# Kernel tuning notes

Hardware: AMD Instinct MI355X
Metric: run time of the kernel (lower is better)

The kernel has to match this reference:

```python
import math
import jax, jax.numpy as jnp
import numpy as np

LOG_NORM = -0.5 * math.log(2.0 * math.pi)  # per-dim gaussian normalizer
HEADS = 4
EM_ITERS = 5


def _mab(x, wq, bq, wk, bk, wv, bv, wo, bo):
    # Set-Transformer SAB(x) = MAB(x, x), ln=False
    B, S, D = x.shape
    dh = D // HEADS
    q = (x @ wq + bq).reshape(B, S, HEADS, dh)
    k = (x @ wk + bk).reshape(B, S, HEADS, dh)
    v = (x @ wv + bv).reshape(B, S, HEADS, dh)
    att = jax.nn.softmax(jnp.einsum('bqhd,bkhd->bhqk', q, k) / math.sqrt(D), axis=-1)
    o = q + jnp.einsum('bhqk,bkhd->bqhd', att, v)
    o = o.reshape(B, S, D)
    return o + jax.nn.relu(o @ wo + bo)


def setup_inputs() -> dict:
    key = jax.random.key(0)
    ks = jax.random.split(key, 16)
    B, S, D, L, K, MC = 16, 256, 512, 64, 20, 10
    s512 = 1.0 / math.sqrt(512.0)
    inp = {
        'H': jax.random.normal(ks[0], (B, S, D), jnp.float32),
        'eps': jax.random.normal(ks[1], (B * S, MC, L), jnp.float32),
        'sab_wq': jax.random.normal(ks[2], (2, D, D), jnp.float32) * s512,
        'sab_bq': jnp.zeros((2, D), jnp.float32),
        'sab_wk': jax.random.normal(ks[3], (2, D, D), jnp.float32) * s512,
        'sab_bk': jnp.zeros((2, D), jnp.float32),
        'sab_wv': jax.random.normal(ks[4], (2, D, D), jnp.float32) * s512,
        'sab_bv': jnp.zeros((2, D), jnp.float32),
        'sab_wo': jax.random.normal(ks[5], (2, D, D), jnp.float32) * s512,
        'sab_bo': jnp.zeros((2, D), jnp.float32),
        'wz': jax.random.normal(ks[6], (D, 2 * L), jnp.float32) * 0.02,
        'bz': jnp.zeros((2 * L,), jnp.float32),
        'w1': jax.random.normal(ks[7], (L, 2 * D), jnp.float32) * (1.0 / math.sqrt(L)),
        'b1': jnp.zeros((2 * D,), jnp.float32),
        'w2': jax.random.normal(ks[8], (2 * D, 2 * D), jnp.float32) * (1.0 / math.sqrt(2 * D)),
        'b2': jnp.zeros((2 * D,), jnp.float32),
        'w3': jax.random.normal(ks[9], (2 * D, D), jnp.float32) * (1.0 / math.sqrt(2 * D)),
        'b3': jnp.zeros((D,), jnp.float32),
    }
    rng = np.random.default_rng(1)
    # component_size distinct indices into the S*MC latent samples, per batch
    inp['init_idx'] = jnp.asarray(
        np.stack([rng.permutation(S * MC)[:K] for _ in range(B)]).astype(np.int32))
    return inp


def reference(H, eps, init_idx, sab_wq, sab_bq, sab_wk, sab_bk, sab_wv, sab_bv,
              sab_wo, sab_bo, wz, bz, w1, b1, w2, b2, w3, b3):
    B, S, D = H.shape
    MC, L = eps.shape[1], eps.shape[2]
    K = init_idx.shape[1]

    # q(z|x): two SABs + linear head
    h = H
    for i in range(2):
        h = _mab(h, sab_wq[i], sab_bq[i], sab_wk[i], sab_bk[i],
                 sab_wv[i], sab_bv[i], sab_wo[i], sab_bo[i])
    stats = h @ wz + bz                                    # [B,S,2L]
    mean, logvar = stats[..., :L], stats[..., L:]
    std = jnp.exp(0.5 * logvar)
    z = mean.reshape(B * S, 1, L) + eps * std.reshape(B * S, 1, L)
    z = z.reshape(B, S, MC, L)
    all_z = z.reshape(B, S * MC, L)                        # [B,N,L]

    # unsupervised EM prior (unit-variance GMM); distances via expansion
    pi = jnp.full((B, K), 1.0 / K, dtype=H.dtype)
    mu = jnp.take_along_axis(all_z, init_idx[:, :, None], axis=1)  # [B,K,L]
    x2 = jnp.sum(all_z * all_z, axis=-1)                   # [B,N]
    for _ in range(EM_ITERS):
        m2 = jnp.sum(mu * mu, axis=-1)                     # [B,K]
        ll = (-0.5 * (x2[:, :, None] - 2.0 * jnp.einsum('bnd,bkd->bnk', all_z, mu)
                      + m2[:, None, :]) + L * LOG_NORM + jnp.log(pi)[:, None, :])
        post = jax.nn.softmax(ll, axis=-1)                 # [B,N,K]
        Nk = post.sum(axis=1)                              # [B,K]
        pi = Nk / Nk.sum(axis=-1, keepdims=True)
        mu = jnp.einsum('bnk,bnd->bkd', post, all_z) / Nk[:, :, None]
    pi = jax.lax.stop_gradient(pi)
    mu = jax.lax.stop_gradient(mu)

    # reconstruction
    zf = z.reshape(-1, L)
    hr = jax.nn.relu(zf @ w1 + b1)
    hr = jax.nn.relu(hr @ w2 + b2)
    hr = jax.nn.relu(hr @ w3 + b3)
    hr = hr.reshape(B, S, MC, D)
    rec_loss = jnp.sum((hr - H[:, :, None, :]) ** 2) / (B * S * MC)

    # KL
    log_qz = jnp.sum(-0.5 * (logvar[:, :, None, :]
                             + (z - mean[:, :, None, :]) ** 2 / jnp.exp(logvar)[:, :, None, :])
                     + LOG_NORM, axis=-1)                  # [B,S,MC]
    z2 = jnp.sum(z * z, axis=-1)                           # [B,S,MC]
    m2 = jnp.sum(mu * mu, axis=-1)                         # [B,K]
    ll = (-0.5 * (z2[..., None] - 2.0 * jnp.einsum('bsmd,bkd->bsmk', z, mu)
                  + m2[:, None, None, :]) + L * LOG_NORM + jnp.log(pi)[:, None, None, :])
    log_pz = jax.scipy.special.logsumexp(ll, axis=-1)      # [B,S,MC]
    kl_loss = jnp.mean(log_qz - log_pz)
    return rec_loss, kl_loss
```

## Files before the change

kernel.cpp:

```cpp
#include <hip/hip_runtime.h>
#include <hip/hip_bf16.h>
#include <math.h>


#define BATCH 16
#define SEQ 256
#define DIM 512
#define NH 4
#define DH 128
#define LD 64
#define KC 20
#define MC 10
#define NPTS 2560
#define BS_TOT 4096
#define NROWS 40960
#define LOG_NORM (-0.9189385332046727f)

typedef __attribute__((ext_vector_type(8))) short bf16x8;
typedef __attribute__((ext_vector_type(4))) float f32x4;
typedef __hip_bfloat16 bf;

__device__ inline float warpReduceSum(float v) {
    for (int o = 32; o > 0; o >>= 1) v += __shfl_down(v, o);
    return v;
}

__device__ inline void async_copy16(const bf* g, bf* l) {
    __builtin_amdgcn_global_load_lds(
        (const __attribute__((address_space(1))) unsigned int*)g,
        (__attribute__((address_space(3))) unsigned int*)l, 16, 0, 0);
}

__device__ inline void split_store(float x, bf* ph, bf* pl, long idx) {
    const bf h = __float2bfloat16(x);
    ph[idx] = h;
    pl[idx] = __float2bfloat16(x - __bfloat162float(h));
}

template<int MODE>
__global__ __launch_bounds__(256, 3)
void gemm3t(const bf* __restrict__ Ah, const bf* __restrict__ Al,
            const bf* __restrict__ Bh, const bf* __restrict__ Bl,
            int K, int lda, int ldb,
            const float* __restrict__ b0, const float* __restrict__ b1v,
            const float* __restrict__ b2v,
            float* __restrict__ outF,
            bf* __restrict__ P1h, bf* __restrict__ P1l,
            bf* __restrict__ P2h, bf* __restrict__ P2l,
            bf* __restrict__ P3h, bf* __restrict__ P3l,
            const bf* __restrict__ Rh, const bf* __restrict__ Rl)
{
    __shared__ __align__(16) char smem[49152];
    float* Xs = (float*)smem;

    const int t = threadIdx.x;
    const int m0 = blockIdx.y * 64, n0 = blockIdx.x * 128;
    const int w = t >> 6, lane = t & 63;
    const int wn = w * 32;
    const int fm = lane & 15, quad = lane >> 4, fk = quad * 8;
    const int srow = t >> 2, scol = (t & 3) * 8;

    f32x4 acc[4][2];
#pragma unroll
    for (int i = 0; i < 4; i++)
#pragma unroll
        for (int j = 0; j < 2; j++) acc[i][j] = (f32x4){0.f, 0.f, 0.f, 0.f};

    const int nk2 = K >> 6;
    for (int kk2 = 0; kk2 < nk2; kk2++) {
#pragma unroll
        for (int h = 0; h < 2; h++) {
            const int kk = kk2 * 2 + h;
            char* base = smem + h * 24576;
            bf* Ash = (bf*)base;
            bf* Asl = (bf*)(base + 4096);
            bf* Bsh = (bf*)(base + 8192);
            bf* Bsl = (bf*)(base + 16384);
            const long ao = (long)(m0 + srow) * lda + kk * 32 + scol;
            const long bo = (long)(n0 + srow) * ldb + kk * 32 + scol;
            async_copy16(Ah + ao, Ash + w * 512);
            async_copy16(Al + ao, Asl + w * 512);
            async_copy16(Bh + bo, Bsh + w * 512);
            async_copy16(Bh + bo + 64L * ldb, Bsh + 2048 + w * 512);
            async_copy16(Bl + bo, Bsl + w * 512);
            async_copy16(Bl + bo + 64L * ldb, Bsl + 2048 + w * 512);
        }
        __syncthreads();

#pragma unroll
        for (int h = 0; h < 2; h++) {
            char* base = smem + h * 24576;
            bf* Ash = (bf*)base;
            bf* Asl = (bf*)(base + 4096);
            bf* Bsh = (bf*)(base + 8192);
            bf* Bsl = (bf*)(base + 16384);
            bf16x8 afh[4], afl[4], bfh[2], bfl[2];
#pragma unroll
            for (int mi = 0; mi < 4; mi++) {
                afh[mi] = *(const bf16x8*)&Ash[(mi * 16 + fm) * 32 + fk];
                afl[mi] = *(const bf16x8*)&Asl[(mi * 16 + fm) * 32 + fk];
            }
#pragma unroll
            for (int ni = 0; ni < 2; ni++) {
                bfh[ni] = *(const bf16x8*)&Bsh[(wn + ni * 16 + fm) * 32 + fk];
                bfl[ni] = *(const bf16x8*)&Bsl[(wn + ni * 16 + fm) * 32 + fk];
            }
#pragma unroll
            for (int mi = 0; mi < 4; mi++)
#pragma unroll
                for (int ni = 0; ni < 2; ni++) {
                    acc[mi][ni] = __builtin_amdgcn_mfma_f32_16x16x32_bf16(
                        afh[mi], bfh[ni], acc[mi][ni], 0, 0, 0);
                    acc[mi][ni] = __builtin_amdgcn_mfma_f32_16x16x32_bf16(
                        afh[mi], bfl[ni], acc[mi][ni], 0, 0, 0);
                    acc[mi][ni] = __builtin_amdgcn_mfma_f32_16x16x32_bf16(
                        afl[mi], bfh[ni], acc[mi][ni], 0, 0, 0);
                }
        }
        __syncthreads();
    }

    const int rl = t >> 2;
    const int cc4 = (t & 3) * 16;

    for (int p = 0; p < 2; p++) {
        if ((w >> 1) == p) {
            const int cb = wn - p * 64;
#pragma unroll
            for (int mi = 0; mi < 4; mi++)
#pragma unroll
                for (int ni = 0; ni < 2; ni++) {
                    const int c = cb + ni * 16 + fm;
#pragma unroll
                    for (int r = 0; r < 4; r++)
                        Xs[(mi * 16 + quad * 4 + r) * 68 + c] = acc[mi][ni][r];
                }
        }
        __syncthreads();

        if (MODE == 0 && n0 >= 1024) {
            const int hh = (n0 >> 7) & 3;
            const int dd = p * 64 + rl;
            const int bb = m0 >> 8;
            const int sb = (m0 & 255) + cc4;
            const float bias = b2v[hh * 128 + dd];
            const long ob = (((long)(bb * NH + hh) * DH + dd) << 8) + sb;
#pragma unroll
            for (int j = 0; j < 2; j++) {
                bf16x8 vh, vl;
#pragma unroll
                for (int i = 0; i < 8; i++) {
                    const float x = Xs[(cc4 + j * 8 + i) * 68 + rl] + bias;
                    const bf h = __float2bfloat16(x);
                    vh[i] = *(const short*)&h;
                    const bf l = __float2bfloat16(x - __bfloat162float(h));
                    vl[i] = *(const short*)&l;
                }
                *(bf16x8*)&P3h[ob + j * 8] = vh;
                *(bf16x8*)&P3l[ob + j * 8] = vl;
            }
        } else {
            float xv[16];
#pragma unroll
            for (int i = 0; i < 4; i++)
                *(float4*)&xv[i * 4] = *(const float4*)&Xs[rl * 68 + cc4 + i * 4];

            if (MODE == 0) {
                const int which = n0 >> 9;
                const int colq = (n0 & 511) + p * 64 + cc4;
                const float* bias = which ? b1v : b0;
                bf* Ph = which ? P2h : P1h;
                bf* Pl = which ? P2l : P1l;
                const long ob = (long)(m0 + rl) * 512 + colq;
#pragma unroll
                for (int j = 0; j < 2; j++) {
                    bf16x8 vh, vl;
#pragma unroll
                    for (int i = 0; i < 8; i++) {
                        const float x = xv[j * 8 + i] + bias[colq + j * 8 + i];
                        const bf h = __float2bfloat16(x); vh[i] = *(const short*)&h;
                        const bf l = __float2bfloat16(x - __bfloat162float(h));
                        vl[i] = *(const short*)&l;
                    }
                    *(bf16x8*)&Ph[ob + j * 8] = vh;
                    *(bf16x8*)&Pl[ob + j * 8] = vl;
                }
            } else if (MODE == 3) {
                const int colg = n0 + p * 64 + cc4;
                const long ob = (long)(m0 + rl) * 512 + colg;
#pragma unroll
                for (int j = 0; j < 2; j++) {
                    const bf16x8 rh = *(const bf16x8*)&Rh[ob + j * 8];
                    const bf16x8 rv = *(const bf16x8*)&Rl[ob + j * 8];
                    bf16x8 vh, vl;
#pragma unroll
                    for (int i = 0; i < 8; i++) {
                        short sh = rh[i], sl = rv[i];
                        float x = fmaxf(xv[j * 8 + i] + b0[colg + j * 8 + i], 0.f)
                                + __bfloat162float(*(const bf*)&sh)
                                + __bfloat162float(*(const bf*)&sl);
                        const bf h = __float2bfloat16(x); vh[i] = *(const short*)&h;
                        const bf l = __float2bfloat16(x - __bfloat162float(h));
                        vl[i] = *(const short*)&l;
                    }
                    *(bf16x8*)&P1h[ob + j * 8] = vh;
                    *(bf16x8*)&P1l[ob + j * 8] = vl;
                }
            } else {
                const int colg = p * 64 + cc4;
                const long ob = (long)(m0 + rl) * 128 + colg;
#pragma unroll
                for (int i = 0; i < 4; i++) {
                    float4 v = *(float4*)&xv[i * 4];
                    v.x += b0[colg + i * 4 + 0];
                    v.y += b0[colg + i * 4 + 1];
                    v.z += b0[colg + i * 4 + 2];
                    v.w += b0[colg + i * 4 + 3];
                    *(float4*)&outF[ob + i * 4] = v;
                }
            }
        }
        __syncthreads();
    }
}

__global__ __launch_bounds__(256)
void attn_fused(const bf* __restrict__ qh, const bf* __restrict__ ql,
                const bf* __restrict__ kh, const bf* __restrict__ kl,
                const bf* __restrict__ vTh, const bf* __restrict__ vTl,
                bf* __restrict__ oh, bf* __restrict__ ol)
{
    __shared__ __align__(16) char smem[43008];
    bf* Qsh = (bf*)smem;            bf* Qsl = (bf*)(smem + 4096);
    bf* Ksh = (bf*)(smem + 8192);   bf* Ksl = (bf*)(smem + 24576);
    bf* Psh = (bf*)smem;            bf* Psl = (bf*)(smem + 4096);
    bf* Vsh = (bf*)(smem + 8192);   bf* Vsl = (bf*)(smem + 16384);
    float (*red)[4]  = (float(*)[4])(smem + 40960);
    float (*red2)[4] = (float(*)[4])(smem + 41984);

    const int t = threadIdx.x;
    const int z = blockIdx.y;
    const int m0 = blockIdx.x * 64;
    const int bb = z >> 2, hh = z & 3;
    const long hOff = (long)bb * 131072 + (long)hh * 128;
    const long vOff = (long)z * 32768;

    const int w = t >> 6, lane = t & 63;
    const int fm = lane & 15;
    const int quad = lane >> 4;
    const int fk = quad * 8;
    const int srow = t >> 2, scol = (t & 3) * 8;

    f32x4 acc[4][4];
#pragma unroll
    for (int i = 0; i < 4; i++)
#pragma unroll
        for (int j = 0; j < 4; j++) acc[i][j] = (f32x4){0.f, 0.f, 0.f, 0.f};

    for (int kk = 0; kk < 4; kk++) {
        const long ao = hOff + (long)(m0 + srow) * 512 + kk * 32 + scol;
        const long bo = hOff + (long)srow * 512 + kk * 32 + scol;
        async_copy16(qh + ao, Qsh + w * 512);
        async_copy16(ql + ao, Qsl + w * 512);
#pragma unroll
        for (int j = 0; j < 4; j++) {
            async_copy16(kh + bo + (long)j * 64 * 512, Ksh + w * 512 + j * 2048);
            async_copy16(kl + bo + (long)j * 64 * 512, Ksl + w * 512 + j * 2048);
        }
        __syncthreads();

        bf16x8 afh[4], afl[4];
#pragma unroll
        for (int mi = 0; mi < 4; mi++) {
            afh[mi] = *(const bf16x8*)&Qsh[(mi * 16 + fm) * 32 + fk];
            afl[mi] = *(const bf16x8*)&Qsl[(mi * 16 + fm) * 32 + fk];
        }
#pragma unroll
        for (int ni = 0; ni < 4; ni++) {
            const bf16x8 bh = *(const bf16x8*)&Ksh[(w * 64 + ni * 16 + fm) * 32 + fk];
            const bf16x8 bl = *(const bf16x8*)&Ksl[(w * 64 + ni * 16 + fm) * 32 + fk];
#pragma unroll
            for (int mi = 0; mi < 4; mi++) {
                acc[mi][ni] = __builtin_amdgcn_mfma_f32_16x16x32_bf16(
                    afh[mi], bh, acc[mi][ni], 0, 0, 0);
                acc[mi][ni] = __builtin_amdgcn_mfma_f32_16x16x32_bf16(
                    afh[mi], bl, acc[mi][ni], 0, 0, 0);
                acc[mi][ni] = __builtin_amdgcn_mfma_f32_16x16x32_bf16(
                    afl[mi], bh, acc[mi][ni], 0, 0, 0);
            }
        }
        __syncthreads();
    }

    const float alpha = 0.044194173824159216f;
#pragma unroll
    for (int mi = 0; mi < 4; mi++)
#pragma unroll
        for (int r = 0; r < 4; r++) {
            float m = -1e30f;
#pragma unroll
            for (int ni = 0; ni < 4; ni++) m = fmaxf(m, acc[mi][ni][r]);
            for (int o = 8; o > 0; o >>= 1) m = fmaxf(m, __shfl_xor(m, o));
            if (fm == 0) red[mi * 16 + quad * 4 + r][w] = m;
        }
    __syncthreads();
    float invr[4][4];
#pragma unroll
    for (int mi = 0; mi < 4; mi++)
#pragma unroll
        for (int r = 0; r < 4; r++) {
            const int rowl = mi * 16 + quad * 4 + r;
            const float mx = fmaxf(fmaxf(red[rowl][0], red[rowl][1]),
                                   fmaxf(red[rowl][2], red[rowl][3]));
            float s = 0.f;
#pragma unroll
            for (int ni = 0; ni < 4; ni++) {
                const float e = __expf((acc[mi][ni][r] - mx) * alpha);
                acc[mi][ni][r] = e;
                s += e;
            }
            for (int o = 8; o > 0; o >>= 1) s += __shfl_xor(s, o);
            if (fm == 0) red2[rowl][w] = s;
        }
    __syncthreads();
#pragma unroll
    for (int mi = 0; mi < 4; mi++)
#pragma unroll
        for (int r = 0; r < 4; r++) {
            const int rowl = mi * 16 + quad * 4 + r;
            invr[mi][r] = 1.f / (red2[rowl][0] + red2[rowl][1] + red2[rowl][2] + red2[rowl][3]);
        }

    f32x4 acc2[4][2];
#pragma unroll
    for (int i = 0; i < 4; i++)
#pragma unroll
        for (int j = 0; j < 2; j++) acc2[i][j] = (f32x4){0.f, 0.f, 0.f, 0.f};

    for (int kc = 0; kc < 8; kc++) {
        if (w == (kc >> 1)) {
            const int nib = (kc & 1) * 2;
#pragma unroll
            for (int mi = 0; mi < 4; mi++)
#pragma unroll
                for (int r = 0; r < 4; r++) {
                    const int row = mi * 16 + quad * 4 + r;
#pragma unroll
                    for (int j = 0; j < 2; j++) {
                        const float p = acc[mi][nib + j][r] * invr[mi][r];
                        const int cc = j * 16 + fm;
                        const bf h = __float2bfloat16(p);
                        Psh[row * 32 + cc] = h;
                        Psl[row * 32 + cc] = __float2bfloat16(p - __bfloat162float(h));
                    }
                }
        }
        const long vo = vOff + (long)srow * 256 + kc * 32 + scol;
        async_copy16(vTh + vo, Vsh + w * 512);
        async_copy16(vTh + vo + 64L * 256, Vsh + w * 512 + 2048);
        async_copy16(vTl + vo, Vsl + w * 512);
        async_copy16(vTl + vo + 64L * 256, Vsl + w * 512 + 2048);
        __syncthreads();

        bf16x8 pfh[4], pfl[4];
#pragma unroll
        for (int mi = 0; mi < 4; mi++) {
            pfh[mi] = *(const bf16x8*)&Psh[(mi * 16 + fm) * 32 + fk];
            pfl[mi] = *(const bf16x8*)&Psl[(mi * 16 + fm) * 32 + fk];
        }
#pragma unroll
        for (int ni = 0; ni < 2; ni++) {
            const bf16x8 vh = *(const bf16x8*)&Vsh[(w * 32 + ni * 16 + fm) * 32 + fk];
            const bf16x8 vl = *(const bf16x8*)&Vsl[(w * 32 + ni * 16 + fm) * 32 + fk];
#pragma unroll
            for (int mi = 0; mi < 4; mi++) {
                acc2[mi][ni] = __builtin_amdgcn_mfma_f32_16x16x32_bf16(
                    pfh[mi], vh, acc2[mi][ni], 0, 0, 0);
                acc2[mi][ni] = __builtin_amdgcn_mfma_f32_16x16x32_bf16(
                    pfh[mi], vl, acc2[mi][ni], 0, 0, 0);
                acc2[mi][ni] = __builtin_amdgcn_mfma_f32_16x16x32_bf16(
                    pfl[mi], vh, acc2[mi][ni], 0, 0, 0);
            }
        }
        __syncthreads();
    }

#pragma unroll
    for (int ni = 0; ni < 2; ni++) {
        const int col = hh * 128 + w * 32 + ni * 16 + fm;
#pragma unroll
        for (int mi = 0; mi < 4; mi++)
#pragma unroll
            for (int r = 0; r < 4; r++) {
                const int row = mi * 16 + quad * 4 + r;
                const long idx = (long)(bb * 256 + m0 + row) * 512 + col;
                const float x = acc2[mi][ni][r]
                    + __bfloat162float(qh[idx]) + __bfloat162float(ql[idx]);
                split_store(x, oh, ol, idx);
            }
    }
}

template<bool SQLOSS>
__global__ __launch_bounds__(256, 3)
void gemm_mfma(const bf* __restrict__ A, const bf* __restrict__ BT,
               bf* __restrict__ C,
               const float* __restrict__ bias,
               const float* __restrict__ Href,
               float* __restrict__ lossAcc,
               int K, int N)
{
    __shared__ __align__(16) char smem[32768];
    bf* Cs  = (bf*)smem;
    __shared__ float redS[4];

    const int t = threadIdx.x;
    const int flat = blockIdx.y * gridDim.x + blockIdx.x;
    const int lane8 = flat & 7;
    const int grp = flat >> 3;
    const int n_blk = grp % gridDim.x;
    const int m_blk = (grp / gridDim.x) * 8 + lane8;
    const int m0 = m_blk * 128, n0 = n_blk * 128;

    const int w = t >> 6, lane = t & 63;
    const int wm = (w >> 1) * 64, wn = (w & 1) * 64;
    const int fm = lane & 15;
    const int quad = lane >> 4;
    const int fk = quad * 8;
    const int srow = t >> 2, scol = (t & 3) * 8;

    f32x4 acc[4][4];
#pragma unroll
    for (int i = 0; i < 4; i++)
#pragma unroll
        for (int j = 0; j < 4; j++) acc[i][j] = (f32x4){0.f, 0.f, 0.f, 0.f};

    const int nk2 = K >> 6;
    for (int kt2 = 0; kt2 < nk2; kt2++) {
#pragma unroll
        for (int h = 0; h < 2; h++) {
            const int kt = kt2 * 2 + h;
            bf* Asg = (bf*)(smem + h * 16384);
            bf* Bsg = (bf*)(smem + h * 16384 + 8192);
            const bf* ga = A + (long)(m0 + srow) * K + kt * 32 + scol;
            const bf* gb = BT + (long)(n0 + srow) * K + kt * 32 + scol;
            async_copy16(ga, Asg + w * 512);
            async_copy16(ga + 64L * K, Asg + 2048 + w * 512);
            async_copy16(gb, Bsg + w * 512);
            async_copy16(gb + 64L * K, Bsg + 2048 + w * 512);
        }
        __syncthreads();

#pragma unroll
        for (int h = 0; h < 2; h++) {
            bf* Asg = (bf*)(smem + h * 16384);
            bf* Bsg = (bf*)(smem + h * 16384 + 8192);
            bf16x8 af[4], bfr[4];
#pragma unroll
            for (int mi = 0; mi < 4; mi++)
                af[mi] = *(const bf16x8*)&Asg[(wm + mi * 16 + fm) * 32 + fk];
#pragma unroll
            for (int ni = 0; ni < 4; ni++)
                bfr[ni] = *(const bf16x8*)&Bsg[(wn + ni * 16 + fm) * 32 + fk];
#pragma unroll
            for (int mi = 0; mi < 4; mi++)
#pragma unroll
                for (int ni = 0; ni < 4; ni++)
                    acc[mi][ni] = __builtin_amdgcn_mfma_f32_16x16x32_bf16(
                        af[mi], bfr[ni], acc[mi][ni], 0, 0, 0);
        }
        __syncthreads();
    }

    if (SQLOSS) {
        float lsum = 0.f;
#pragma unroll
        for (int ni = 0; ni < 4; ni++) {
            const int col = n0 + wn + ni * 16 + fm;
            const float b = bias[col];
#pragma unroll
            for (int mi = 0; mi < 4; mi++)
#pragma unroll
                for (int r = 0; r < 4; r++) {
                    const int row = m0 + wm + mi * 16 + quad * 4 + r;
                    const float x = fmaxf(acc[mi][ni][r] + b, 0.f);
                    const float d = x - Href[(long)(row / MC) * DIM + col];
                    lsum = fmaf(d, d, lsum);
                }
        }
        lsum = warpReduceSum(lsum);
        if (lane == 0) redS[w] = lsum;
        __syncthreads();
        if (t == 0) atomicAdd(lossAcc, redS[0] + redS[1] + redS[2] + redS[3]);
    } else {
        for (int hf = 0; hf < 2; hf++) {
            if ((w >> 1) == hf) {
#pragma unroll
                for (int ni = 0; ni < 4; ni++) {
                    const int c = wn + ni * 16 + fm;
                    const float bv = bias[n0 + c];
#pragma unroll
                    for (int mi = 0; mi < 4; mi++)
#pragma unroll
                        for (int r = 0; r < 4; r++) {
                            const float x = fmaxf(acc[mi][ni][r] + bv, 0.f);
                            Cs[(mi * 16 + quad * 4 + r) * 136 + c] = __float2bfloat16(x);
                        }
                }
            }
            __syncthreads();
            const int rl2 = t >> 2, cc2 = (t & 3) * 32;
            const long ob = (long)(m0 + hf * 64 + rl2) * N + n0 + cc2;
#pragma unroll
            for (int j = 0; j < 4; j++)
                *(bf16x8*)&C[ob + j * 8] = *(const bf16x8*)&Cs[rl2 * 136 + cc2 + j * 8];
            __syncthreads();
        }
    }
}

__global__ __launch_bounds__(512, 2)
void gemm_8ph(const bf* __restrict__ A, const bf* __restrict__ BT,
              bf* __restrict__ C, const float* __restrict__ bias,
              int K, int N)
{
    __shared__ __align__(16) char smem8[135168];
    bf* lds = (bf*)smem8;

    const int t = threadIdx.x;
    const int w = t >> 6, lane = t & 63;
    const int wr = w >> 2, wc = w & 3;
    const int fm = lane & 15, quad = lane >> 4, fm7 = fm & 7;

    const int NNB = N >> 8;
    const int cpx = gridDim.x >> 3;
    const int bid = blockIdx.x;
    const int swz = (bid & 7) * cpx + (bid >> 3);
    const int m0 = (swz / NNB) * 256;
    const int n0 = (swz % NNB) * 256;

#define OffA(b, h) ((b) * 16384 + (h) * 8192)
#define OffB(b, h) (32768 + (b) * 16384 + (h) * 8192)

    const int r8 = lane >> 3;
    const int c8 = (lane & 7) ^ r8;
    const long ldk = (long)K;
    const bf* pA0 = A  + (long)(m0 + w * 16 + r8) * ldk + c8 * 8;
    const bf* pA1 = pA0 + 128L * ldk;
    const bf* pB0 = BT + (long)(n0 + w * 16 + r8) * ldk + c8 * 8;
    const bf* pB1 = pB0 + 128L * ldk;

#define STAGE(BASE, KT, OFF) do {                                        \
        const bf* _g = (BASE) + (KT) * 64;                               \
        async_copy16(_g, &lds[(OFF) + w * 1024]);                        \
        async_copy16(_g + (ldk << 3), &lds[(OFF) + w * 1024 + 512]);     \
    } while (0)

    bf16x8 fa[4][2], fb0[2][2], fb1[2][2];
    f32x4 acc[8][4];
#pragma unroll
    for (int i = 0; i < 8; i++)
#pragma unroll
        for (int j = 0; j < 4; j++) acc[i][j] = (f32x4){0.f, 0.f, 0.f, 0.f};

#define READ_A(b, qm) do {                                               \
        const bf* Ab = &lds[OffA(b, wr)];                                \
        _Pragma("unroll")                                                \
        for (int mi2 = 0; mi2 < 4; mi2++) {                              \
            const int lr = (qm) * 64 + mi2 * 16 + fm;                    \
            fa[mi2][0] = *(const bf16x8*)&Ab[lr * 64 + ((quad) ^ fm7) * 8];      \
            fa[mi2][1] = *(const bf16x8*)&Ab[lr * 64 + ((4 + quad) ^ fm7) * 8];  \
        }                                                                \
    } while (0)

#define READ_B(b, qn, FB) do {                                           \
        const bf* Bb = &lds[OffB(b, wc >> 1)];                           \
        _Pragma("unroll")                                                \
        for (int ni2 = 0; ni2 < 2; ni2++) {                              \
            const int lr = (wc & 1) * 64 + ((qn) * 2 + ni2) * 16 + fm;   \
            FB[ni2][0] = *(const bf16x8*)&Bb[lr * 64 + ((quad) ^ fm7) * 8];      \
            FB[ni2][1] = *(const bf16x8*)&Bb[lr * 64 + ((4 + quad) ^ fm7) * 8];  \
        }                                                                \
    } while (0)

#define MFMA_Q(qm, qn, FB) do {                                          \
        _Pragma("unroll")                                                \
        for (int mi2 = 0; mi2 < 4; mi2++)                                \
            _Pragma("unroll")                                            \
            for (int ni2 = 0; ni2 < 2; ni2++) {                          \
                acc[(qm) * 4 + mi2][(qn) * 2 + ni2] =                    \
                    __builtin_amdgcn_mfma_f32_16x16x32_bf16(             \
                        fa[mi2][0], FB[ni2][0],                          \
                        acc[(qm) * 4 + mi2][(qn) * 2 + ni2], 0, 0, 0);   \
                acc[(qm) * 4 + mi2][(qn) * 2 + ni2] =                    \
                    __builtin_amdgcn_mfma_f32_16x16x32_bf16(             \
                        fa[mi2][1], FB[ni2][1],                          \
                        acc[(qm) * 4 + mi2][(qn) * 2 + ni2], 0, 0, 0);   \
            }                                                            \
    } while (0)

#define BAR()  __builtin_amdgcn_s_barrier()
#define LGKM() asm volatile("s_waitcnt lgkmcnt(0)" ::: "memory")
#define VM4()  asm volatile("s_waitcnt vmcnt(4)" ::: "memory")
#define PRIO1() __builtin_amdgcn_s_setprio(1)
#define PRIO0() __builtin_amdgcn_s_setprio(0)

    const int NKT = K >> 6;
    const int NIT = NKT >> 1;

    STAGE(pB0, 0, OffB(0, 0));
    STAGE(pB1, 0, OffB(0, 1));
    STAGE(pA0, 0, OffA(0, 0));
    STAGE(pA1, 0, OffA(0, 1));
    STAGE(pB0, 1, OffB(1, 0));
    STAGE(pB1, 1, OffB(1, 1));
    VM4();
    BAR();

    for (int it = 0; it < NIT; it++) {
        const int t1 = 2 * it + 1;
        const int t2 = (2 * it + 2 < NKT) ? 2 * it + 2 : NKT - 1;
        const int t3 = (2 * it + 3 < NKT) ? 2 * it + 3 : NKT - 1;

        READ_A(0, 0);
        READ_B(0, 0, fb0);
        STAGE(pA0, t1, OffA(1, 0));
        BAR(); LGKM();
        PRIO1(); MFMA_Q(0, 0, fb0); PRIO0();
        BAR();
        READ_B(0, 1, fb1);
        STAGE(pA1, t1, OffA(1, 1));
        BAR(); LGKM();
        PRIO1(); MFMA_Q(0, 1, fb1); PRIO0();
        BAR();
        READ_A(0, 1);
        STAGE(pB0, t2, OffB(0, 0));
        BAR(); LGKM();
        PRIO1(); MFMA_Q(1, 1, fb1); PRIO0();
        BAR();
        STAGE(pB1, t2, OffB(0, 1));
        BAR(); LGKM();
        PRIO1(); MFMA_Q(1, 0, fb0); PRIO0();
        VM4();
        BAR();
        READ_A(1, 0);
        READ_B(1, 0, fb0);
        STAGE(pA0, t2, OffA(0, 0));
        BAR(); LGKM();
        PRIO1(); MFMA_Q(0, 0, fb0); PRIO0();
        BAR();
        READ_B(1, 1, fb1);
        STAGE(pA1, t2, OffA(0, 1));
        BAR(); LGKM();
        PRIO1(); MFMA_Q(0, 1, fb1); PRIO0();
        BAR();
        READ_A(1, 1);
        STAGE(pB0, t3, OffB(1, 0));
        BAR(); LGKM();
        PRIO1(); MFMA_Q(1, 1, fb1); PRIO0();
        BAR();
        STAGE(pB1, t3, OffB(1, 1));
        BAR(); LGKM();
        PRIO1(); MFMA_Q(1, 0, fb0); PRIO0();
        VM4();
        BAR();
    }

    __syncthreads();

    bf* Cs = (bf*)smem8;
#pragma unroll
    for (int ni = 0; ni < 4; ni++) {
        const int c = wc * 64 + ni * 16 + fm;
        const float bv = bias[n0 + c];
#pragma unroll
        for (int mi = 0; mi < 8; mi++)
#pragma unroll
            for (int r = 0; r < 4; r++) {
                const int row = wr * 128 + mi * 16 + quad * 4 + r;
                Cs[row * 264 + c] = __float2bfloat16(fmaxf(acc[mi][ni][r] + bv, 0.f));
            }
    }
    __syncthreads();

    const int srow = t >> 1;
    const int scb = (t & 1) * 128;
    const long ob = (long)(m0 + srow) * N + n0 + scb;
    const bf* src = &Cs[srow * 264 + scb];
#pragma unroll
    for (int j = 0; j < 16; j++)
        *(bf16x8*)&C[ob + j * 8] = *(const bf16x8*)&src[j * 8];

#undef OffA
#undef OffB
#undef STAGE
#undef READ_A
#undef READ_B
#undef MFMA_Q
#undef BAR
#undef LGKM
#undef VM4
#undef PRIO1
#undef PRIO0
}

__global__ void conv_all(
    const float* __restrict__ H, bf* __restrict__ h0h, bf* __restrict__ h0l,
    const float* __restrict__ wq, const float* __restrict__ wk,
    const float* __restrict__ wv, const float* __restrict__ wo,
    bf* __restrict__ qkvTh0, bf* __restrict__ qkvTl0,
    bf* __restrict__ woTh0, bf* __restrict__ woTl0,
    bf* __restrict__ qkvTh1, bf* __restrict__ qkvTl1,
    bf* __restrict__ woTh1, bf* __restrict__ woTl1,
    const float* __restrict__ wz, bf* __restrict__ wzTh, bf* __restrict__ wzTl,
    const float* __restrict__ w1, bf* __restrict__ w1T,
    const float* __restrict__ w2, bf* __restrict__ w2T,
    const float* __restrict__ w3, bf* __restrict__ w3T,
    float* __restrict__ scal, float* __restrict__ msP, float* __restrict__ nkP)
{
    const int t = threadIdx.x;
    if (blockIdx.x == 0 && t < 16) scal[t] = 0.f;
    const int gidx = blockIdx.x * 256 + t;
    if (gidx < 2097152) {
        const float x = H[gidx];
        const bf h = __float2bfloat16(x);
        h0h[gidx] = h;
        h0l[gidx] = __float2bfloat16(x - __bfloat162float(h));
        return;
    }
    const int idx = gidx - 2097152;
    if (idx < 2097152) {
        const int layer = idx >> 20;
        const int seg = (idx >> 18) & 3;
        const int r = idx & 262143;
        const int k = r >> 9, n = r & 511;
        const float* src = ((seg == 0) ? wq : (seg == 1) ? wk : (seg == 2) ? wv : wo)
                           + (long)layer * 262144;
        const float x = src[r];
        const bf h = __float2bfloat16(x);
        const bf l = __float2bfloat16(x - __bfloat162float(h));
        if (seg < 3) {
            const long o = (long)(seg * 512 + n) * 512 + k;
            if (layer == 0) { qkvTh0[o] = h; qkvTl0[o] = l; }
            else            { qkvTh1[o] = h; qkvTl1[o] = l; }
        } else {
            const long o = (long)n * 512 + k;
            if (layer == 0) { woTh0[o] = h; woTl0[o] = l; }
            else            { woTh1[o] = h; woTl1[o] = l; }
        }
    } else if (idx < 2162688) {
        const int i = idx - 2097152;
        const int k = i >> 7, n = i & 127;
        const float x = wz[i];
        const bf h = __float2bfloat16(x);
        wzTh[(long)n * 512 + k] = h;
        wzTl[(long)n * 512 + k] = __float2bfloat16(x - __bfloat162float(h));
    } else if (idx < 2228224) {
        const int i = idx - 2162688;
        const int k = i >> 10, n = i & 1023;
        w1T[(long)n * 64 + k] = __float2bfloat16(w1[i]);
    } else if (idx < 3276800) {
        const int i = idx - 2228224;
        const int k = i >> 10, n = i & 1023;
        w2T[(long)n * 1024 + k] = __float2bfloat16(w2[i]);
    } else if (idx < 3801088) {
        const int i = idx - 3276800;
        const int k = i >> 9, n = i & 511;
        w3T[(long)n * 1024 + k] = __float2bfloat16(w3[i]);
    } else if (idx < 3903488) {
        msP[20480 + (idx - 3801088)] = 0.f;
    } else if (idx < 3905088) {
        nkP[320 + (idx - 3903488)] = 0.f;
    }
}

__global__ __launch_bounds__(256)
void zgen(const float* __restrict__ stats, const float* __restrict__ eps,
          float* __restrict__ z, bf* __restrict__ z16)
{
    const int idx = blockIdx.x * 256 + threadIdx.x;
    const int bs = idx / 160;
    const int r = idx % 160;
    const int l4 = r % 16;
    const float4 e = ((const float4*)eps)[idx];
    const float4 mn = ((const float4*)stats)[bs * 32 + l4];
    const float4 lv = ((const float4*)stats)[bs * 32 + 16 + l4];
    float4 zz;
    zz.x = fmaf(e.x, expf(0.5f * lv.x), mn.x);
    zz.y = fmaf(e.y, expf(0.5f * lv.y), mn.y);
    zz.z = fmaf(e.z, expf(0.5f * lv.z), mn.z);
    zz.w = fmaf(e.w, expf(0.5f * lv.w), mn.w);
    ((float4*)z)[idx] = zz;
    bf* zp = z16 + (long)idx * 4;
    zp[0] = __float2bfloat16(zz.x);
    zp[1] = __float2bfloat16(zz.y);
    zp[2] = __float2bfloat16(zz.z);
    zp[3] = __float2bfloat16(zz.w);
}

__global__ void em_init(const float* __restrict__ z, const int* __restrict__ init_idx,
                        float* __restrict__ ms0, float* __restrict__ nk0)
{
    const int b = blockIdx.x, t = threadIdx.x;
    for (int i = t; i < KC * LD; i += 256) {
        const int k = i >> 6, l = i & 63;
        const int idx = init_idx[b * KC + k];
        ms0[b * KC * LD + i] = z[((long)b * NPTS + idx) * LD + l];
    }
    if (t < KC) nk0[b * KC + t] = 1.f;
}

__global__ __launch_bounds__(256)
void em_step(const float* __restrict__ z,
             const float* __restrict__ msIn, const float* __restrict__ nkIn,
             float* __restrict__ msOut, float* __restrict__ nkOut)
{
    __shared__ float muS[KC][65];
    __shared__ float m2lp[KC];
    __shared__ float NkU[KC];
    __shared__ float postS[KC][256];
    __shared__ float NkS[KC];

    const int tile = blockIdx.x, b = blockIdx.y, t = threadIdx.x;
    const int lane = t & 63, w = t >> 6;

    if (t < KC) NkU[t] = nkIn[b * KC + t];
    __syncthreads();
    for (int i = t; i < KC * LD; i += 256)
        muS[i >> 6][i & 63] = msIn[b * KC * LD + i] / NkU[i >> 6];
    __syncthreads();
    if (t < KC) {
        float s = 0.f;
        for (int l = 0; l < LD; l++) { const float m = muS[t][l]; s = fmaf(m, m, s); }
        float sn = 0.f;
        for (int k = 0; k < KC; k++) sn += NkU[k];
        m2lp[t] = -0.5f * s + logf(NkU[t] / sn);
    }
    __syncthreads();

    const long n = (long)tile * 256 + t;
    const float* zr = &z[((long)b * NPTS + n) * LD];
    float acc[KC];
#pragma unroll
    for (int k = 0; k < KC; k++) acc[k] = 0.f;
#pragma unroll
    for (int l4 = 0; l4 < 16; l4++) {
        const float4 zv = ((const float4*)zr)[l4];
#pragma unroll
        for (int k = 0; k < KC; k++) {
            acc[k] = fmaf(zv.x, muS[k][l4 * 4 + 0], acc[k]);
            acc[k] = fmaf(zv.y, muS[k][l4 * 4 + 1], acc[k]);
            acc[k] = fmaf(zv.z, muS[k][l4 * 4 + 2], acc[k]);
            acc[k] = fmaf(zv.w, muS[k][l4 * 4 + 3], acc[k]);
        }
    }
    float mx = -1e30f;
    float llv[KC];
#pragma unroll
    for (int k = 0; k < KC; k++) { llv[k] = acc[k] + m2lp[k]; mx = fmaxf(mx, llv[k]); }
    float s = 0.f;
#pragma unroll
    for (int k = 0; k < KC; k++) { llv[k] = expf(llv[k] - mx); s += llv[k]; }
    const float inv = 1.f / s;
#pragma unroll
    for (int k = 0; k < KC; k++) postS[k][t] = llv[k] * inv;
    __syncthreads();

#pragma unroll
    for (int kk = 0; kk < 5; kk++) {
        const int k = w * 5 + kk;
        float p = postS[k][lane] + postS[k][lane + 64] + postS[k][lane + 128] + postS[k][lane + 192];
        p = warpReduceSum(p);
        if (lane == 0) NkS[k] = p;
    }
    __syncthreads();

    const float* zb = &z[((long)b * NPTS + (long)tile * 256) * LD];
#pragma unroll
    for (int j = 0; j < 5; j++) {
        const int o = t + j * 256;
        const int k = o >> 6, l = o & 63;
        float sacc = 0.f;
        for (int n2 = 0; n2 < 256; n2++)
            sacc = fmaf(postS[k][n2], zb[n2 * LD + l], sacc);
        atomicAdd(&msOut[b * KC * LD + o], sacc);
    }
    if (t < KC) atomicAdd(&nkOut[b * KC + t], NkS[t]);
}

__global__ __launch_bounds__(256)
void kl_kernel(const float* __restrict__ z, const float* __restrict__ stats,
               const float* __restrict__ eps,
               const float* __restrict__ msIn, const float* __restrict__ nkIn,
               float* __restrict__ klAcc)
{
    __shared__ float muS[KC][65];
    __shared__ float m2lp[KC];
    __shared__ float NkU[KC];
    __shared__ float redS[4];

    const int tile = blockIdx.x, b = blockIdx.y, t = threadIdx.x;

    if (t < KC) NkU[t] = nkIn[b * KC + t];
    __syncthreads();
    for (int i = t; i < KC * LD; i += 256)
        muS[i >> 6][i & 63] = msIn[b * KC * LD + i] / NkU[i >> 6];
    __syncthreads();
    if (t < KC) {
        float s = 0.f;
        for (int l = 0; l < LD; l++) { const float m = muS[t][l]; s = fmaf(m, m, s); }
        float sn = 0.f;
        for (int k = 0; k < KC; k++) sn += NkU[k];
        m2lp[t] = -0.5f * s + logf(NkU[t] / sn);
    }
    __syncthreads();

    const int n = tile * 256 + t;
    const int sidx = n / MC, m = n % MC;
    const long bs = (long)b * SEQ + sidx;
    const float* zr = &z[((long)b * NPTS + n) * LD];

    float acc[KC];
#pragma unroll
    for (int k = 0; k < KC; k++) acc[k] = 0.f;
    float x2 = 0.f;
#pragma unroll
    for (int l4 = 0; l4 < 16; l4++) {
        const float4 zv = ((const float4*)zr)[l4];
        x2 = fmaf(zv.x, zv.x, fmaf(zv.y, zv.y, fmaf(zv.z, zv.z, fmaf(zv.w, zv.w, x2))));
#pragma unroll
        for (int k = 0; k < KC; k++) {
            acc[k] = fmaf(zv.x, muS[k][l4 * 4 + 0], acc[k]);
            acc[k] = fmaf(zv.y, muS[k][l4 * 4 + 1], acc[k]);
            acc[k] = fmaf(zv.z, muS[k][l4 * 4 + 2], acc[k]);
            acc[k] = fmaf(zv.w, muS[k][l4 * 4 + 3], acc[k]);
        }
    }
    float mx = -1e30f;
    float llv[KC];
#pragma unroll
    for (int k = 0; k < KC; k++) { llv[k] = acc[k] + m2lp[k]; mx = fmaxf(mx, llv[k]); }
    float s = 0.f;
#pragma unroll
    for (int k = 0; k < KC; k++) s += expf(llv[k] - mx);
    const float log_pz = -0.5f * x2 + mx + logf(s) + LD * LOG_NORM;

    const float* lvr = &stats[bs * 128 + 64];
    const float* er = &eps[(bs * MC + m) * LD];
    float slv = 0.f, se2 = 0.f;
#pragma unroll
    for (int l4 = 0; l4 < 16; l4++) {
        const float4 lv = ((const float4*)lvr)[l4];
        slv += lv.x + lv.y + lv.z + lv.w;
        const float4 e = ((const float4*)er)[l4];
        se2 = fmaf(e.x, e.x, fmaf(e.y, e.y, fmaf(e.z, e.z, fmaf(e.w, e.w, se2))));
    }
    const float log_qz = -0.5f * (slv + se2) + LD * LOG_NORM;

    float v = log_qz - log_pz;
    v = warpReduceSum(v);
    if ((t & 63) == 0) redS[t >> 6] = v;
    __syncthreads();
    if (t == 0) atomicAdd(klAcc, redS[0] + redS[1] + redS[2] + redS[3]);
}

__global__ void finalize(const float* __restrict__ scal, float* __restrict__ out)
{
    if (threadIdx.x == 0) {
        out[0] = scal[0] * (1.f / (float)NROWS);
        out[1] = scal[1] * (1.f / (float)NROWS);
    }
}

extern "C" void kernel_launch(void* const* d_in, const int* in_sizes, int n_in,
                              void* d_out, int out_size, void* d_ws, size_t ws_size,
                              hipStream_t stream)
{
    const float* H   = (const float*)d_in[0];
    const float* eps = (const float*)d_in[1];
    const float* wq  = (const float*)d_in[2];
    const float* bq  = (const float*)d_in[3];
    const float* wk  = (const float*)d_in[4];
    const float* bk  = (const float*)d_in[5];
    const float* wv  = (const float*)d_in[6];
    const float* bv  = (const float*)d_in[7];
    const float* wo  = (const float*)d_in[8];
    const float* bo  = (const float*)d_in[9];
    const float* wz  = (const float*)d_in[10];
    const float* bz  = (const float*)d_in[11];
    const float* w1  = (const float*)d_in[12];
    const float* b1  = (const float*)d_in[13];
    const float* w2  = (const float*)d_in[14];
    const float* b2  = (const float*)d_in[15];
    const float* w3  = (const float*)d_in[16];
    const float* b3  = (const float*)d_in[17];
    const int* init_idx = (const int*)d_in[18];
    float* out = (float*)d_out;
    float* wsf = (float*)d_ws;

    const long o_scal  = 0;
    const long o_nk    = 1024;
    const long o_ms    = 4096;
    const long o_st    = 131072;
    const long o_zb    = 655360;
    const long o_z16   = 3276800;
    const long o_q     = 4587520;
    const long o_k     = 6684672;
    const long o_vT    = 8781824;
    const long o_o     = 10878976;
    const long o_h1    = 12976128;
    const long o_qkvT0 = 15073280;
    const long o_woT0  = 15859712;
    const long o_qkvT1 = 16121856;
    const long o_woT1  = 16908288;
    const long o_wzT   = 17170432;
    const long o_w1T   = 17235968;
    const long o_w2T   = 17268736;
    const long o_w3T   = 17793024;
    const long o_d1    = 18055168;
    const long o_d2    = 39026688;

    const long PL = (long)BS_TOT * DIM;
    bf* qh  = (bf*)(wsf + o_q);   bf* ql  = qh + PL;
    bf* kh  = (bf*)(wsf + o_k);   bf* kl_ = kh + PL;
    bf* vTh = (bf*)(wsf + o_vT);  bf* vTl = vTh + PL;
    bf* oh  = (bf*)(wsf + o_o);   bf* ol  = oh + PL;
    bf* h1h = (bf*)(wsf + o_h1);  bf* h1l = h1h + PL;
    bf* h2h = qh;                 bf* h2l = ql;
    bf* qkvTh0 = (bf*)(wsf + o_qkvT0); bf* qkvTl0 = qkvTh0 + 1536L * 512;
    bf* woTh0  = (bf*)(wsf + o_woT0);  bf* woTl0  = woTh0 + 512L * 512;
    bf* qkvTh1 = (bf*)(wsf + o_qkvT1); bf* qkvTl1 = qkvTh1 + 1536L * 512;
    bf* woTh1  = (bf*)(wsf + o_woT1);  bf* woTl1  = woTh1 + 512L * 512;
    bf* wzTh = (bf*)(wsf + o_wzT);     bf* wzTl = wzTh + 128L * 512;
    bf* w1T = (bf*)(wsf + o_w1T);
    bf* w2T = (bf*)(wsf + o_w2T);
    bf* w3T = (bf*)(wsf + o_w3T);
    bf* z16 = (bf*)(wsf + o_z16);
    bf* d1  = (bf*)(wsf + o_d1);
    bf* d2  = (bf*)(wsf + o_d2);
    float* st = wsf + o_st;
    float* zb = wsf + o_zb;
    float* scal = wsf + o_scal;
    float* msP = wsf + o_ms;
    float* nkP = wsf + o_nk;

    const dim3 blk(256);

    conv_all<<<23447, blk, 0, stream>>>(
        H, h1h, h1l,
        wq, wk, wv, wo,
        qkvTh0, qkvTl0, woTh0, woTl0,
        qkvTh1, qkvTl1, woTh1, woTl1,
        wz, wzTh, wzTl, w1, w1T, w2, w2T, w3, w3T,
        scal, msP, nkP);

    for (int i = 0; i < 2; i++) {
        const long boff = (long)i * DIM;
        bf* qkh = i ? qkvTh1 : qkvTh0;  bf* qkl = i ? qkvTl1 : qkvTl0;
        bf* wh  = i ? woTh1 : woTh0;    bf* wl  = i ? woTl1 : woTl0;

        gemm3t<0><<<dim3(12, 64), blk, 0, stream>>>(
            h1h, h1l, qkh, qkl, 512, 512, 512,
            bq + boff, bk + boff, bv + boff, nullptr,
            qh, ql, kh, kl_, vTh, vTl, nullptr, nullptr);
        attn_fused<<<dim3(4, 64), blk, 0, stream>>>(qh, ql, kh, kl_, vTh, vTl, oh, ol);
        bf* houth = (i == 0) ? h1h : h2h;
        bf* houtl = (i == 0) ? h1l : h2l;
        gemm3t<3><<<dim3(4, 64), blk, 0, stream>>>(
            oh, ol, wh, wl, 512, 512, 512,
            bo + boff, nullptr, nullptr, nullptr,
            houth, houtl, nullptr, nullptr, nullptr, nullptr, oh, ol);
    }

    gemm3t<4><<<dim3(1, 64), blk, 0, stream>>>(
        h2h, h2l, wzTh, wzTl, 512, 512, 512,
        bz, nullptr, nullptr, st,
        nullptr, nullptr, nullptr, nullptr, nullptr, nullptr, nullptr, nullptr);

    zgen<<<2560, blk, 0, stream>>>(st, eps, zb, z16);

    gemm_mfma<false><<<dim3(8, 320), blk, 0, stream>>>(
        z16, w1T, d1, b1, nullptr, nullptr, 64, 1024);
    gemm_8ph<<<dim3(640), dim3(512), 0, stream>>>(d1, w2T, d2, b2, 1024, 1024);
    gemm_mfma<true><<<dim3(4, 320), blk, 0, stream>>>(
        d2, w3T, nullptr, b3, H, scal + 0, 1024, 512);

    em_init<<<16, blk, 0, stream>>>(zb, init_idx, msP, nkP);
    for (int it = 0; it < 5; it++) {
        em_step<<<dim3(10, 16), blk, 0, stream>>>(
            zb,
            msP + (long)it * 16 * KC * LD, nkP + (long)it * 16 * KC,
            msP + (long)(it + 1) * 16 * KC * LD, nkP + (long)(it + 1) * 16 * KC);
    }
    kl_kernel<<<dim3(10, 16), blk, 0, stream>>>(
        zb, st, eps,
        msP + 5L * 16 * KC * LD, nkP + 5L * 16 * KC, scal + 1);

    finalize<<<1, 64, 0, stream>>>(scal, out);
}
```

Measured before the change: 685.2 us.

## Double-buffer MFMA fragment registers and remove extra barriers in GEMM main loop

Result: no change. 681.1 us (-0.6%).

```diff
diff --git a/kernel.cpp b/kernel.cpp
--- a/kernel.cpp
+++ b/kernel.cpp
@@ -556,113 +556,106 @@
         async_copy16(_g + (ldk << 3), &lds[(OFF) + w * 1024 + 512]);     \
     } while (0)
 
-    bf16x8 fa[4][2], fb0[2][2], fb1[2][2];
+    bf16x8 faA[4][2], faB[4][2], fb1v[2][2], fb0A[2][2], fb0B[2][2];
     f32x4 acc[8][4];
 #pragma unroll
     for (int i = 0; i < 8; i++)
 #pragma unroll
         for (int j = 0; j < 4; j++) acc[i][j] = (f32x4){0.f, 0.f, 0.f, 0.f};
 
-#define READ_A(b, qm) do {                                               \
+#define READ_FA(DST, b, QM) do {                                         \
         const bf* Ab = &lds[OffA(b, wr)];                                \
         _Pragma("unroll")                                                \
         for (int mi2 = 0; mi2 < 4; mi2++) {                              \
-            const int lr = (qm) * 64 + mi2 * 16 + fm;                    \
-            fa[mi2][0] = *(const bf16x8*)&Ab[lr * 64 + ((quad) ^ fm7) * 8];      \
-            fa[mi2][1] = *(const bf16x8*)&Ab[lr * 64 + ((4 + quad) ^ fm7) * 8];  \
+            const int lr = (QM) * 64 + mi2 * 16 + fm;                    \
+            DST[mi2][0] = *(const bf16x8*)&Ab[lr * 64 + ((quad) ^ fm7) * 8];      \
+            DST[mi2][1] = *(const bf16x8*)&Ab[lr * 64 + ((4 + quad) ^ fm7) * 8];  \
         }                                                                \
     } while (0)
 
-#define READ_B(b, qn, FB) do {                                           \
+#define READ_FB(DST, b, QN) do {                                         \
         const bf* Bb = &lds[OffB(b, wc >> 1)];                           \
         _Pragma("unroll")                                                \
         for (int ni2 = 0; ni2 < 2; ni2++) {                              \
-            const int lr = (wc & 1) * 64 + ((qn) * 2 + ni2) * 16 + fm;   \
-            FB[ni2][0] = *(const bf16x8*)&Bb[lr * 64 + ((quad) ^ fm7) * 8];      \
-            FB[ni2][1] = *(const bf16x8*)&Bb[lr * 64 + ((4 + quad) ^ fm7) * 8];  \
+            const int lr = (wc & 1) * 64 + (QN) * 32 + ni2 * 16 + fm;    \
+            DST[ni2][0] = *(const bf16x8*)&Bb[lr * 64 + ((quad) ^ fm7) * 8];      \
+            DST[ni2][1] = *(const bf16x8*)&Bb[lr * 64 + ((4 + quad) ^ fm7) * 8];  \
         }                                                                \
     } while (0)
 
-#define MFMA_Q(qm, qn, FB) do {                                          \
+#define MFMA_Q(FA, FB, QM, QN) do {                                      \
         _Pragma("unroll")                                                \
         for (int mi2 = 0; mi2 < 4; mi2++)                                \
             _Pragma("unroll")                                            \
             for (int ni2 = 0; ni2 < 2; ni2++) {                          \
-                acc[(qm) * 4 + mi2][(qn) * 2 + ni2] =                    \
+                acc[(QM) * 4 + mi2][(QN) * 2 + ni2] =                    \
                     __builtin_amdgcn_mfma_f32_16x16x32_bf16(             \
-                        fa[mi2][0], FB[ni2][0],                          \
-                        acc[(qm) * 4 + mi2][(qn) * 2 + ni2], 0, 0, 0);   \
-                acc[(qm) * 4 + mi2][(qn) * 2 + ni2] =                    \
+                        FA[mi2][0], FB[ni2][0],                          \
+                        acc[(QM) * 4 + mi2][(QN) * 2 + ni2], 0, 0, 0);   \
+                acc[(QM) * 4 + mi2][(QN) * 2 + ni2] =                    \
                     __builtin_amdgcn_mfma_f32_16x16x32_bf16(             \
-                        fa[mi2][1], FB[ni2][1],                          \
-                        acc[(qm) * 4 + mi2][(qn) * 2 + ni2], 0, 0, 0);   \
+                        FA[mi2][1], FB[ni2][1],                          \
+                        acc[(QM) * 4 + mi2][(QN) * 2 + ni2], 0, 0, 0);   \
             }                                                            \
     } while (0)
 
 #define BAR()  __builtin_amdgcn_s_barrier()
-#define LGKM() asm volatile("s_waitcnt lgkmcnt(0)" ::: "memory")
-#define VM4()  asm volatile("s_waitcnt vmcnt(4)" ::: "memory")
+#define VMW2() asm volatile("s_waitcnt vmcnt(2)" ::: "memory")
+#define VMW4() asm volatile("s_waitcnt vmcnt(4)" ::: "memory")
 #define PRIO1() __builtin_amdgcn_s_setprio(1)
 #define PRIO0() __builtin_amdgcn_s_setprio(0)
 
     const int NKT = K >> 6;
     const int NIT = NKT >> 1;
 
+    STAGE(pA0, 0, OffA(0, 0));
+    STAGE(pA1, 0, OffA(0, 1));
     STAGE(pB0, 0, OffB(0, 0));
     STAGE(pB1, 0, OffB(0, 1));
-    STAGE(pA0, 0, OffA(0, 0));
-    STAGE(pA1, 0, OffA(0, 1));
     STAGE(pB0, 1, OffB(1, 0));
     STAGE(pB1, 1, OffB(1, 1));
-    VM4();
+    VMW4();
     BAR();
+    READ_FB(fb0A, 0, 0);
 
     for (int it = 0; it < NIT; it++) {
         const int t1 = 2 * it + 1;
         const int t2 = (2 * it + 2 < NKT) ? 2 * it + 2 : NKT - 1;
         const int t3 = (2 * it + 3 < NKT) ? 2 * it + 3 : NKT - 1;
 
-        READ_A(0, 0);
-        READ_B(0, 0, fb0);
+        READ_FA(faA, 0, 0);
+        READ_FB(fb1v, 0, 1);
         STAGE(pA0, t1, OffA(1, 0));
-        BAR(); LGKM();
-        PRIO1(); MFMA_Q(0, 0, fb0); PRIO0();
+        PRIO1(); MFMA_Q(faA, fb0A, 0, 0); PRIO0();
         BAR();
-        READ_B(0, 1, fb1);
         STAGE(pA1, t1, OffA(1, 1));
-        BAR(); LGKM();
-        PRIO1(); MFMA_Q(0, 1, fb1); PRIO0();
+        PRIO1(); MFMA_Q(faA, fb1v, 0, 1); PRIO0();
         BAR();
-        READ_A(0, 1);
+        READ_FA(faB, 0, 1);
         STAGE(pB0, t2, OffB(0, 0));
-        BAR(); LGKM();
-        PRIO1(); MFMA_Q(1, 1, fb1); PRIO0();
+        PRIO1(); MFMA_Q(faB, fb1v, 1, 1); PRIO0();
+        VMW2();
         BAR();
+        READ_FB(fb0B, 1, 0);
         STAGE(pB1, t2, OffB(0, 1));
-        BAR(); LGKM();
-        PRIO1(); MFMA_Q(1, 0, fb0); PRIO0();
-        VM4();
+        PRIO1(); MFMA_Q(faB, fb0A, 1, 0); PRIO0();
         BAR();
-        READ_A(1, 0);
-        READ_B(1, 0, fb0);
+        READ_FA(faA, 1, 0);
+        READ_FB(fb1v, 1, 1);
         STAGE(pA0, t2, OffA(0, 0));
-        BAR(); LGKM();
-        PRIO1(); MFMA_Q(0, 0, fb0); PRIO0();
+        PRIO1(); MFMA_Q(faA, fb0B, 0, 0); PRIO0();
         BAR();
-        READ_B(1, 1, fb1);
         STAGE(pA1, t2, OffA(0, 1));
-        BAR(); LGKM();
-        PRIO1(); MFMA_Q(0, 1, fb1); PRIO0();
+        PRIO1(); MFMA_Q(faA, fb1v, 0, 1); PRIO0();
         BAR();
-        READ_A(1, 1);
+        READ_FA(faB, 1, 1);
         STAGE(pB0, t3, OffB(1, 0));
-        BAR(); LGKM();
-        PRIO1(); MFMA_Q(1, 1, fb1); PRIO0();
+        PRIO1(); MFMA_Q(faB, fb1v, 1, 1); PRIO0();
+        VMW2();
         BAR();
+        READ_FB(fb0A, 0, 0);
         STAGE(pB1, t3, OffB(1, 1));
-        BAR(); LGKM();
-        PRIO1(); MFMA_Q(1, 0, fb0); PRIO0();
-        VM4();
+        PRIO1(); MFMA_Q(faB, fb0B, 1, 0); PRIO0();
         BAR();
     }
 
@@ -694,12 +687,12 @@
 #undef OffA
 #undef OffB
 #undef STAGE
-#undef READ_A
-#undef READ_B
+#undef READ_FA
+#undef READ_FB
 #undef MFMA_Q
 #undef BAR
-#undef LGKM
-#undef VM4
+#undef VMW2
+#undef VMW4
 #undef PRIO1
 #undef PRIO0
 }
```
